# Performance work log

Hardware: AMD Instinct MI355X
Metric: run time of the kernel (lower is better)

Reference implementation:

```python
import jax, jax.numpy as jnp
import numpy as np

B, N, C = 2, 512, 256


def setup_inputs() -> dict:
    key = jax.random.key(0)
    ks = jax.random.split(key, 6)
    s = 0.02
    return {
        "x": jax.random.normal(ks[0], (B, N, C), dtype=jnp.float32),
        "Wq": jax.random.normal(ks[1], (C, C), dtype=jnp.float32) * s,
        "Wk": jax.random.normal(ks[2], (C, C), dtype=jnp.float32) * s,
        "Wv": jax.random.normal(ks[3], (C, C), dtype=jnp.float32) * s,
        "Wp": jax.random.normal(ks[4], (C, C), dtype=jnp.float32) * s,
        "bp": jax.random.normal(ks[5], (C,), dtype=jnp.float32) * s,
    }


def reference(x, Wq, Wk, Wv, Wp, bp):
    # q,k,v: [B,N,C]; torch Linear(no bias) = x @ W.T
    q = jnp.einsum("bnc,dc->bnd", x, Wq)
    k = jnp.einsum("bnc,dc->bnd", x, Wk)
    v = jnp.einsum("bnc,dc->bnd", x, Wv)
    # additive score: sum_c relu(q_i + k_j)  -> [B,N,N]
    score = jax.nn.relu(q[:, :, None, :] + k[:, None, :, :]).sum(axis=-1)
    attn = jax.nn.softmax(score, axis=-1)  # [B,N,N] over keys j
    out = jnp.einsum("bij,bjc->bic", attn, v)  # weighted v sum
    out = jnp.einsum("bnc,dc->bnd", out, Wp) + bp  # proj (with bias)
    return out
```

## Files before the change

kernel.cpp:

```cpp
#include <hip/hip_runtime.h>
#include <hip/hip_bf16.h>


#define QSTR 132
#define VSTR 260

__global__ __launch_bounds__(256, 2) void gemm_qkv(
    const float* __restrict__ x,
    const float* __restrict__ Wq, const float* __restrict__ Wk, const float* __restrict__ Wv,
    float4* __restrict__ qt4, float* __restrict__ k, float* __restrict__ v,
    float* __restrict__ Ksp)
{
    const int z = blockIdx.z;
    const float* W = (z == 0) ? Wq : ((z == 1) ? Wk : Wv);
    const int row0 = blockIdx.x * 32;
    const int d0   = blockIdx.y * 64;

    __shared__ __attribute__((aligned(16))) float AT[2][32][36];
    __shared__ __attribute__((aligned(16))) float WT[2][32][68];

    const int tid = threadIdx.x;
    const int ty = tid >> 4, tx = tid & 15;
    const int ar = tid >> 3, ac = (tid & 7) * 4;
    const int wd = tid >> 2, wc = (tid & 3) * 8;

    const float* xg = x + (size_t)(row0 + ar) * 256 + ac;
    const float* wg = W + (size_t)(d0 + wd) * 256 + wc;

    float4 ra  = *(const float4*)xg;
    float4 rw0 = *(const float4*)wg;
    float4 rw1 = *(const float4*)(wg + 4);

    AT[0][ac+0][ar]=ra.x;  AT[0][ac+1][ar]=ra.y;  AT[0][ac+2][ar]=ra.z;  AT[0][ac+3][ar]=ra.w;
    WT[0][wc+0][wd]=rw0.x; WT[0][wc+1][wd]=rw0.y; WT[0][wc+2][wd]=rw0.z; WT[0][wc+3][wd]=rw0.w;
    WT[0][wc+4][wd]=rw1.x; WT[0][wc+5][wd]=rw1.y; WT[0][wc+6][wd]=rw1.z; WT[0][wc+7][wd]=rw1.w;
    __syncthreads();

    float acc[2][4] = {};

#pragma unroll 1
    for (int kc = 0; kc < 8; ++kc) {
        const int cur = kc & 1;
        if (kc < 7) {
            ra  = *(const float4*)(xg + (kc + 1) * 32);
            rw0 = *(const float4*)(wg + (kc + 1) * 32);
            rw1 = *(const float4*)(wg + (kc + 1) * 32 + 4);
        }
#pragma unroll
        for (int c = 0; c < 32; ++c) {
            float2 a  = *(const float2*)&AT[cur][c][ty * 2];
            float4 w4 = *(const float4*)&WT[cur][c][tx * 4];
            acc[0][0] += a.x * w4.x; acc[0][1] += a.x * w4.y;
            acc[0][2] += a.x * w4.z; acc[0][3] += a.x * w4.w;
            acc[1][0] += a.y * w4.x; acc[1][1] += a.y * w4.y;
            acc[1][2] += a.y * w4.z; acc[1][3] += a.y * w4.w;
        }
        if (kc < 7) {
            const int nx = cur ^ 1;
            AT[nx][ac+0][ar]=ra.x;  AT[nx][ac+1][ar]=ra.y;  AT[nx][ac+2][ar]=ra.z;  AT[nx][ac+3][ar]=ra.w;
            WT[nx][wc+0][wd]=rw0.x; WT[nx][wc+1][wd]=rw0.y; WT[nx][wc+2][wd]=rw0.z; WT[nx][wc+3][wd]=rw0.w;
            WT[nx][wc+4][wd]=rw1.x; WT[nx][wc+5][wd]=rw1.y; WT[nx][wc+6][wd]=rw1.z; WT[nx][wc+7][wd]=rw1.w;
            __syncthreads();
        }
    }

    if (z == 0) {
#pragma unroll
        for (int rr = 0; rr < 2; ++rr)
            qt4[(size_t)(d0 / 4 + tx) * 1024 + row0 + ty * 2 + rr] =
                make_float4(acc[rr][0], acc[rr][1], acc[rr][2], acc[rr][3]);
    } else {
        float* out = (z == 1) ? k : v;
#pragma unroll
        for (int rr = 0; rr < 2; ++rr)
            *(float4*)&out[(size_t)(row0 + ty * 2 + rr) * 256 + d0 + tx * 4] =
                make_float4(acc[rr][0], acc[rr][1], acc[rr][2], acc[rr][3]);
        if (z == 1) {
#pragma unroll
            for (int rr = 0; rr < 2; ++rr) {
                float kp = acc[rr][0] + acc[rr][1] + acc[rr][2] + acc[rr][3];
#pragma unroll
                for (int d = 1; d < 16; d <<= 1) kp += __shfl_xor(kp, d, 16);
                if (tx == 0)
                    Ksp[(size_t)(d0 >> 6) * 1024 + row0 + ty * 2 + rr] = kp;
            }
        }
    }
}

__global__ __launch_bounds__(512) void attn_partial(
    const float4* __restrict__ qt4, const float* __restrict__ kk,
    const float* __restrict__ vv, const float* __restrict__ Ksp,
    float4* __restrict__ pacc4, float* __restrict__ ml)
{
    const int it = blockIdx.x;
    const int js = blockIdx.y;
    const int b  = it >> 3;
    const int irow0 = it * 64;
    const int jrow0 = b * 512 + js * 32;

    __shared__ __attribute__((aligned(16))) float qbuf[64 * QSTR];
    __shared__ __attribute__((aligned(16))) float kbuf[32 * QSTR];
    __shared__ float sL[32][65];
    __shared__ float pl[32][65];

    const int t = threadIdx.x;
    const int w = t >> 6;
    const int l = t & 63;
    const int j0 = w * 4;

    float s[4] = {0.f, 0.f, 0.f, 0.f};

    for (int h = 0; h < 2; ++h) {
#pragma unroll
        for (int u = 0; u < 4; ++u) {
            int idx = u * 512 + t;
            int c4 = idx >> 6, row = idx & 63;
            *(float4*)&qbuf[row * QSTR + c4 * 4] =
                qt4[(size_t)(h * 32 + c4) * 1024 + irow0 + row];
        }
#pragma unroll
        for (int u = 0; u < 2; ++u) {
            int idx = u * 512 + t;
            int row = idx >> 5, c4 = idx & 31;
            *(float4*)&kbuf[row * QSTR + c4 * 4] =
                *(const float4*)&kk[(size_t)(jrow0 + row) * 256 + h * 128 + c4 * 4];
        }
        __syncthreads();

        const float* qrow = &qbuf[l * QSTR];
        const float* k0p = &kbuf[(j0 + 0) * QSTR];
        const float* k1p = &kbuf[(j0 + 1) * QSTR];
        const float* k2p = &kbuf[(j0 + 2) * QSTR];
        const float* k3p = &kbuf[(j0 + 3) * QSTR];

        float4 Aqa,Aqb,Ak0a,Ak0b,Ak1a,Ak1b,Ak2a,Ak2b,Ak3a,Ak3b;
        float4 Bqa,Bqb,Bk0a,Bk0b,Bk1a,Bk1b,Bk2a,Bk2b,Bk3a,Bk3b;

#define LDCH(P, c) \
        P##qa  = *(const float4*)(qrow + (c)); P##qb  = *(const float4*)(qrow + (c) + 4); \
        P##k0a = *(const float4*)(k0p + (c)); P##k0b = *(const float4*)(k0p + (c) + 4); \
        P##k1a = *(const float4*)(k1p + (c)); P##k1b = *(const float4*)(k1p + (c) + 4); \
        P##k2a = *(const float4*)(k2p + (c)); P##k2b = *(const float4*)(k2p + (c) + 4); \
        P##k3a = *(const float4*)(k3p + (c)); P##k3b = *(const float4*)(k3p + (c) + 4);
#define CMPJ(jj, QA, QB, KA, KB) \
        s[jj] += fabsf(QA.x + KA.x); s[jj] += fabsf(QA.y + KA.y); \
        s[jj] += fabsf(QA.z + KA.z); s[jj] += fabsf(QA.w + KA.w); \
        s[jj] += fabsf(QB.x + KB.x); s[jj] += fabsf(QB.y + KB.y); \
        s[jj] += fabsf(QB.z + KB.z); s[jj] += fabsf(QB.w + KB.w);
#define CMPALL(P) \
        CMPJ(0, P##qa, P##qb, P##k0a, P##k0b) CMPJ(1, P##qa, P##qb, P##k1a, P##k1b) \
        CMPJ(2, P##qa, P##qb, P##k2a, P##k2b) CMPJ(3, P##qa, P##qb, P##k3a, P##k3b)

        LDCH(A, 0)
#pragma unroll 1
        for (int c0 = 0; c0 < 128; c0 += 16) {
            LDCH(B, c0 + 8)
            CMPALL(A)
            int cn = (c0 + 16) & 127;
            LDCH(A, cn)
            CMPALL(B)
        }
        __syncthreads();
    }

    const int jbase = jrow0 + j0;
    float sc[4];
#pragma unroll
    for (int jj = 0; jj < 4; ++jj) {
        float ks = Ksp[jbase + jj] + Ksp[1024 + jbase + jj]
                 + Ksp[2048 + jbase + jj] + Ksp[3072 + jbase + jj];
        sc[jj] = 0.5f * (s[jj] + ks);
        sL[j0 + jj][l] = sc[jj];
    }

#pragma unroll
    for (int u = 0; u < 4; ++u) {
        int idx = u * 512 + t;
        int row = idx >> 6, c4 = idx & 63;
        *(float4*)&qbuf[row * VSTR + c4 * 4] =
            *(const float4*)&vv[(size_t)(jrow0 + row) * 256 + c4 * 4];
    }
    __syncthreads();

    float m = -1e30f;
#pragma unroll 8
    for (int j = 0; j < 32; ++j) m = fmaxf(m, sL[j][l]);
#pragma unroll
    for (int jj = 0; jj < 4; ++jj)
        pl[j0 + jj][l] = __expf(sc[jj] - m);
    __syncthreads();

    if (w == 0) {
        float lsum = 0.f;
#pragma unroll 8
        for (int j = 0; j < 32; ++j) lsum += pl[j][l];
        *(float2*)&ml[((size_t)(irow0 + l) * 16 + js) * 2] = make_float2(m, lsum);
    }

#define PVACC(P, V0, V1, V2, V3) \
        acc[0]  += P * V0.x; acc[1]  += P * V0.y; acc[2]  += P * V0.z; acc[3]  += P * V0.w; \
        acc[4]  += P * V1.x; acc[5]  += P * V1.y; acc[6]  += P * V1.z; acc[7]  += P * V1.w; \
        acc[8]  += P * V2.x; acc[9]  += P * V2.y; acc[10] += P * V2.z; acc[11] += P * V2.w; \
        acc[12] += P * V3.x; acc[13] += P * V3.y; acc[14] += P * V3.z; acc[15] += P * V3.w;
#define LDV(P, jj) \
        P##p0 = pl[jj][l];        P##p1 = pl[(jj) + 1][l]; \
        P##v0 = *(const float4*)(vb + (jj) * VSTR);      P##v1 = *(const float4*)(vb + (jj) * VSTR + 4); \
        P##v2 = *(const float4*)(vb + (jj) * VSTR + 8);  P##v3 = *(const float4*)(vb + (jj) * VSTR + 12); \
        P##w0 = *(const float4*)(vb + ((jj)+1) * VSTR);     P##w1 = *(const float4*)(vb + ((jj)+1) * VSTR + 4); \
        P##w2 = *(const float4*)(vb + ((jj)+1) * VSTR + 8); P##w3 = *(const float4*)(vb + ((jj)+1) * VSTR + 12);

#pragma unroll 1
    for (int pass = 0; pass < 2; ++pass) {
        const int cb = w * 32 + pass * 16;
        const float* vb = &qbuf[cb];
        float acc[16];
#pragma unroll
        for (int i = 0; i < 16; ++i) acc[i] = 0.f;

        float Ap0, Ap1, Bp0, Bp1;
        float4 Av0,Av1,Av2,Av3, Aw0,Aw1,Aw2,Aw3;
        float4 Bv0,Bv1,Bv2,Bv3, Bw0,Bw1,Bw2,Bw3;
        LDV(A, 0)
#pragma unroll 1
        for (int j = 0; j < 32; j += 4) {
            LDV(B, j + 2)
            PVACC(Ap0, Av0, Av1, Av2, Av3)
            PVACC(Ap1, Aw0, Aw1, Aw2, Aw3)
            int jn = (j + 4) & 31;
            LDV(A, jn)
            PVACC(Bp0, Bv0, Bv1, Bv2, Bv3)
            PVACC(Bp1, Bw0, Bw1, Bw2, Bw3)
        }
        float4* pout = pacc4 + (((size_t)it * 16 + js) * 64 + (cb >> 2)) * 64 + l;
        pout[0]   = make_float4(acc[0],  acc[1],  acc[2],  acc[3]);
        pout[64]  = make_float4(acc[4],  acc[5],  acc[6],  acc[7]);
        pout[128] = make_float4(acc[8],  acc[9],  acc[10], acc[11]);
        pout[192] = make_float4(acc[12], acc[13], acc[14], acc[15]);
    }
}

__global__ __launch_bounds__(256) void combine(
    const float4* __restrict__ pacc4, const float* __restrict__ ml, float* __restrict__ OT)
{
    const int it = blockIdx.x;
    const int cs = blockIdx.y;
    const int t  = threadIdx.x;
    const int il = t & 63, cq = t >> 6;
    const int row = it * 64 + il;
    const int c4g = cs * 4 + cq;

    float mv[16], lv[16], M = -1e30f;
#pragma unroll
    for (int s = 0; s < 16; ++s) {
        float2 e = *(const float2*)&ml[((size_t)row * 16 + s) * 2];
        mv[s] = e.x; lv[s] = e.y; M = fmaxf(M, e.x);
    }
    float L = 0.f;
    float4 o = make_float4(0.f, 0.f, 0.f, 0.f);
#pragma unroll
    for (int s = 0; s < 16; ++s) {
        float wgt = __expf(mv[s] - M);
        L += wgt * lv[s];
        float4 pv = pacc4[(((size_t)it * 16 + s) * 64 + c4g) * 64 + il];
        o.x += wgt * pv.x; o.y += wgt * pv.y; o.z += wgt * pv.z; o.w += wgt * pv.w;
    }
    float inv = 1.f / L;
    OT[(size_t)(c4g * 4 + 0) * 1024 + row] = o.x * inv;
    OT[(size_t)(c4g * 4 + 1) * 1024 + row] = o.y * inv;
    OT[(size_t)(c4g * 4 + 2) * 1024 + row] = o.z * inv;
    OT[(size_t)(c4g * 4 + 3) * 1024 + row] = o.w * inv;
}

__global__ __launch_bounds__(256, 2) void gemm_bias(
    const float* __restrict__ OT, const float* __restrict__ W,
    const float* __restrict__ bias, float* __restrict__ out)
{
    const int row0 = blockIdx.x * 32;
    const int d0   = blockIdx.y * 64;

    __shared__ __attribute__((aligned(16))) float AT[2][32][36];
    __shared__ __attribute__((aligned(16))) float WT[2][32][68];

    const int tid = threadIdx.x;
    const int ty = tid >> 4, tx = tid & 15;
    const int acR = tid >> 3, arQ = (tid & 7) * 4;
    const int wd = tid >> 2, wc = (tid & 3) * 8;

    const float* ag = OT + (size_t)acR * 1024 + row0 + arQ;
    const float* wg = W + (size_t)(d0 + wd) * 256 + wc;

    float4 ra  = *(const float4*)ag;
    float4 rw0 = *(const float4*)wg;
    float4 rw1 = *(const float4*)(wg + 4);

    *(float4*)&AT[0][acR][arQ] = ra;
    WT[0][wc+0][wd]=rw0.x; WT[0][wc+1][wd]=rw0.y; WT[0][wc+2][wd]=rw0.z; WT[0][wc+3][wd]=rw0.w;
    WT[0][wc+4][wd]=rw1.x; WT[0][wc+5][wd]=rw1.y; WT[0][wc+6][wd]=rw1.z; WT[0][wc+7][wd]=rw1.w;
    __syncthreads();

    float acc[2][4] = {};

#pragma unroll 1
    for (int kc = 0; kc < 8; ++kc) {
        const int cur = kc & 1;
        if (kc < 7) {
            ra  = *(const float4*)(ag + (size_t)(kc + 1) * 32 * 1024);
            rw0 = *(const float4*)(wg + (kc + 1) * 32);
            rw1 = *(const float4*)(wg + (kc + 1) * 32 + 4);
        }
#pragma unroll
        for (int c = 0; c < 32; ++c) {
            float2 a  = *(const float2*)&AT[cur][c][ty * 2];
            float4 w4 = *(const float4*)&WT[cur][c][tx * 4];
            acc[0][0] += a.x * w4.x; acc[0][1] += a.x * w4.y;
            acc[0][2] += a.x * w4.z; acc[0][3] += a.x * w4.w;
            acc[1][0] += a.y * w4.x; acc[1][1] += a.y * w4.y;
            acc[1][2] += a.y * w4.z; acc[1][3] += a.y * w4.w;
        }
        if (kc < 7) {
            const int nx = cur ^ 1;
            *(float4*)&AT[nx][acR][arQ] = ra;
            WT[nx][wc+0][wd]=rw0.x; WT[nx][wc+1][wd]=rw0.y; WT[nx][wc+2][wd]=rw0.z; WT[nx][wc+3][wd]=rw0.w;
            WT[nx][wc+4][wd]=rw1.x; WT[nx][wc+5][wd]=rw1.y; WT[nx][wc+6][wd]=rw1.z; WT[nx][wc+7][wd]=rw1.w;
            __syncthreads();
        }
    }
    float4 bb = *(const float4*)&bias[d0 + tx * 4];
#pragma unroll
    for (int rr = 0; rr < 2; ++rr) {
        float4 o = make_float4(acc[rr][0] + bb.x, acc[rr][1] + bb.y,
                               acc[rr][2] + bb.z, acc[rr][3] + bb.w);
        *(float4*)&out[(size_t)(row0 + ty * 2 + rr) * 256 + d0 + tx * 4] = o;
    }
}

extern "C" void kernel_launch(void* const* d_in, const int* in_sizes, int n_in,
                              void* d_out, int out_size, void* d_ws, size_t ws_size,
                              hipStream_t stream) {
    const float* x  = (const float*)d_in[0];
    const float* Wq = (const float*)d_in[1];
    const float* Wk = (const float*)d_in[2];
    const float* Wv = (const float*)d_in[3];
    const float* Wp = (const float*)d_in[4];
    const float* bp = (const float*)d_in[5];
    float* out = (float*)d_out;
    (void)ws_size; (void)in_sizes; (void)n_in; (void)out_size;

    float* ws = (float*)d_ws;
    const size_t BNC = (size_t)2 * 512 * 256;
    float4* qt4 = (float4*)ws;
    float* k    = ws + BNC;
    float* v    = k + BNC;
    float* OT   = v + BNC;
    float* Ksp  = OT + BNC;
    float4* pacc4 = (float4*)(Ksp + 4 * 1024);
    float* mlb  = (float*)(pacc4 + (size_t)16 * 16 * 64 * 64);

    gemm_qkv<<<dim3(32, 4, 3), 256, 0, stream>>>(x, Wq, Wk, Wv, qt4, k, v, Ksp);
    attn_partial<<<dim3(16, 16), 512, 0, stream>>>(qt4, k, v, Ksp, pacc4, mlb);
    combine<<<dim3(16, 16), 256, 0, stream>>>(pacc4, mlb, OT);
    gemm_bias<<<dim3(32, 4), 256, 0, stream>>>(OT, Wp, bp, out);
}
```

Baseline: 61.14 us.

## Fold output projection into value weights and fuse PV with projection

Precomputes Wvp = Wp·Wv so that the V GEMM directly yields projected values. The attention kernel now writes only normalized-partial probabilities P^T plus max/sum stats, and a new pv_proj kernel applies softmax rescaling on the fly while computing P·Vp plus bias. This removes the separate combine and projection GEMM kernels and the large partial-accumulator buffer. In exchange it adds a small weight GEMM launch per call and a 512x1024 probability matrix round-trip through memory.

Measured after the change: 62.16 us. No clear change (+1.7%).

```diff
diff --git a/kernel.cpp b/kernel.cpp
--- a/kernel.cpp
+++ b/kernel.cpp
@@ -3,16 +3,55 @@
 
 
 #define QSTR 132
-#define VSTR 260
+
+__global__ __launch_bounds__(256) void wvp_gemm(
+    const float* __restrict__ Wp, const float* __restrict__ Wv, float* __restrict__ Wvp)
+{
+    const int row0 = blockIdx.x * 32;
+    const int e0   = blockIdx.y * 64;
+
+    __shared__ __attribute__((aligned(16))) float AT[32][36];
+    __shared__ __attribute__((aligned(16))) float BT[32][68];
+
+    const int t = threadIdx.x;
+    const int ty = t >> 4, tx = t & 15;
+    float acc[2][4] = {};
+
+    for (int c0 = 0; c0 < 256; c0 += 32) {
+        {
+            int r = t >> 3, cb = (t & 7) * 4;
+            float4 a = *(const float4*)&Wp[(size_t)(row0 + r) * 256 + c0 + cb];
+            AT[cb+0][r]=a.x; AT[cb+1][r]=a.y; AT[cb+2][r]=a.z; AT[cb+3][r]=a.w;
+        }
+        {
+            int cc = t >> 3, ec = (t & 7) * 8;
+            *(float4*)&BT[cc][ec]     = *(const float4*)&Wv[(size_t)(c0 + cc) * 256 + e0 + ec];
+            *(float4*)&BT[cc][ec + 4] = *(const float4*)&Wv[(size_t)(c0 + cc) * 256 + e0 + ec + 4];
+        }
+        __syncthreads();
+#pragma unroll
+        for (int c = 0; c < 32; ++c) {
+            float2 a  = *(const float2*)&AT[c][ty * 2];
+            float4 w4 = *(const float4*)&BT[c][tx * 4];
+            acc[0][0]+=a.x*w4.x; acc[0][1]+=a.x*w4.y; acc[0][2]+=a.x*w4.z; acc[0][3]+=a.x*w4.w;
+            acc[1][0]+=a.y*w4.x; acc[1][1]+=a.y*w4.y; acc[1][2]+=a.y*w4.z; acc[1][3]+=a.y*w4.w;
+        }
+        __syncthreads();
+    }
+#pragma unroll
+    for (int rr = 0; rr < 2; ++rr)
+        *(float4*)&Wvp[(size_t)(row0 + ty * 2 + rr) * 256 + e0 + tx * 4] =
+            make_float4(acc[rr][0], acc[rr][1], acc[rr][2], acc[rr][3]);
+}
 
 __global__ __launch_bounds__(256, 2) void gemm_qkv(
     const float* __restrict__ x,
-    const float* __restrict__ Wq, const float* __restrict__ Wk, const float* __restrict__ Wv,
-    float4* __restrict__ qt4, float* __restrict__ k, float* __restrict__ v,
+    const float* __restrict__ Wq, const float* __restrict__ Wk, const float* __restrict__ Wvp,
+    float4* __restrict__ qt4, float* __restrict__ k, float* __restrict__ Vp,
     float* __restrict__ Ksp)
 {
     const int z = blockIdx.z;
-    const float* W = (z == 0) ? Wq : ((z == 1) ? Wk : Wv);
+    const float* W = (z == 0) ? Wq : ((z == 1) ? Wk : Wvp);
     const int row0 = blockIdx.x * 32;
     const int d0   = blockIdx.y * 64;
 
@@ -50,10 +89,8 @@
         for (int c = 0; c < 32; ++c) {
             float2 a  = *(const float2*)&AT[cur][c][ty * 2];
             float4 w4 = *(const float4*)&WT[cur][c][tx * 4];
-            acc[0][0] += a.x * w4.x; acc[0][1] += a.x * w4.y;
-            acc[0][2] += a.x * w4.z; acc[0][3] += a.x * w4.w;
-            acc[1][0] += a.y * w4.x; acc[1][1] += a.y * w4.y;
-            acc[1][2] += a.y * w4.z; acc[1][3] += a.y * w4.w;
+            acc[0][0]+=a.x*w4.x; acc[0][1]+=a.x*w4.y; acc[0][2]+=a.x*w4.z; acc[0][3]+=a.x*w4.w;
+            acc[1][0]+=a.y*w4.x; acc[1][1]+=a.y*w4.y; acc[1][2]+=a.y*w4.z; acc[1][3]+=a.y*w4.w;
         }
         if (kc < 7) {
             const int nx = cur ^ 1;
@@ -70,7 +107,7 @@
             qt4[(size_t)(d0 / 4 + tx) * 1024 + row0 + ty * 2 + rr] =
                 make_float4(acc[rr][0], acc[rr][1], acc[rr][2], acc[rr][3]);
     } else {
-        float* out = (z == 1) ? k : v;
+        float* out = (z == 1) ? k : Vp;
 #pragma unroll
         for (int rr = 0; rr < 2; ++rr)
             *(float4*)&out[(size_t)(row0 + ty * 2 + rr) * 256 + d0 + tx * 4] =
@@ -88,10 +125,9 @@
     }
 }
 
-__global__ __launch_bounds__(512) void attn_partial(
+__global__ __launch_bounds__(512) void attn_score(
     const float4* __restrict__ qt4, const float* __restrict__ kk,
-    const float* __restrict__ vv, const float* __restrict__ Ksp,
-    float4* __restrict__ pacc4, float* __restrict__ ml)
+    const float* __restrict__ Ksp, float* __restrict__ PT, float* __restrict__ ml)
 {
     const int it = blockIdx.x;
     const int js = blockIdx.y;
@@ -101,8 +137,8 @@
 
     __shared__ __attribute__((aligned(16))) float qbuf[64 * QSTR];
     __shared__ __attribute__((aligned(16))) float kbuf[32 * QSTR];
-    __shared__ float sL[32][65];
-    __shared__ float pl[32][65];
+    __shared__ float smax[8][65];
+    __shared__ float psum[8][65];
 
     const int t = threadIdx.x;
     const int w = t >> 6;
@@ -171,168 +207,109 @@
         float ks = Ksp[jbase + jj] + Ksp[1024 + jbase + jj]
                  + Ksp[2048 + jbase + jj] + Ksp[3072 + jbase + jj];
         sc[jj] = 0.5f * (s[jj] + ks);
-        sL[j0 + jj][l] = sc[jj];
-    }
-
-#pragma unroll
-    for (int u = 0; u < 4; ++u) {
-        int idx = u * 512 + t;
-        int row = idx >> 6, c4 = idx & 63;
-        *(float4*)&qbuf[row * VSTR + c4 * 4] =
-            *(const float4*)&vv[(size_t)(jrow0 + row) * 256 + c4 * 4];
-    }
-    __syncthreads();
-
-    float m = -1e30f;
-#pragma unroll 8
-    for (int j = 0; j < 32; ++j) m = fmaxf(m, sL[j][l]);
-#pragma unroll
-    for (int jj = 0; jj < 4; ++jj)
-        pl[j0 + jj][l] = __expf(sc[jj] - m);
+    }
+    smax[w][l] = fmaxf(fmaxf(sc[0], sc[1]), fmaxf(sc[2], sc[3]));
+    __syncthreads();
+
+    float m = smax[0][l];
+#pragma unroll
+    for (int ww = 1; ww < 8; ++ww) m = fmaxf(m, smax[ww][l]);
+
+    float ps = 0.f;
+#pragma unroll
+    for (int jj = 0; jj < 4; ++jj) {
+        float p = __expf(sc[jj] - m);
+        ps += p;
+        PT[(size_t)(js * 32 + j0 + jj) * 1024 + irow0 + l] = p;
+    }
+    psum[w][l] = ps;
     __syncthreads();
 
     if (w == 0) {
         float lsum = 0.f;
-#pragma unroll 8
-        for (int j = 0; j < 32; ++j) lsum += pl[j][l];
+#pragma unroll
+        for (int ww = 0; ww < 8; ++ww) lsum += psum[ww][l];
         *(float2*)&ml[((size_t)(irow0 + l) * 16 + js) * 2] = make_float2(m, lsum);
     }
-
-#define PVACC(P, V0, V1, V2, V3) \
-        acc[0]  += P * V0.x; acc[1]  += P * V0.y; acc[2]  += P * V0.z; acc[3]  += P * V0.w; \
-        acc[4]  += P * V1.x; acc[5]  += P * V1.y; acc[6]  += P * V1.z; acc[7]  += P * V1.w; \
-        acc[8]  += P * V2.x; acc[9]  += P * V2.y; acc[10] += P * V2.z; acc[11] += P * V2.w; \
-        acc[12] += P * V3.x; acc[13] += P * V3.y; acc[14] += P * V3.z; acc[15] += P * V3.w;
-#define LDV(P, jj) \
-        P##p0 = pl[jj][l];        P##p1 = pl[(jj) + 1][l]; \
-        P##v0 = *(const float4*)(vb + (jj) * VSTR);      P##v1 = *(const float4*)(vb + (jj) * VSTR + 4); \
-        P##v2 = *(const float4*)(vb + (jj) * VSTR + 8);  P##v3 = *(const float4*)(vb + (jj) * VSTR + 12); \
-        P##w0 = *(const float4*)(vb + ((jj)+1) * VSTR);     P##w1 = *(const float4*)(vb + ((jj)+1) * VSTR + 4); \
-        P##w2 = *(const float4*)(vb + ((jj)+1) * VSTR + 8); P##w3 = *(const float4*)(vb + ((jj)+1) * VSTR + 12);
+}
+
+__global__ __launch_bounds__(256) void pv_proj(
+    const float* __restrict__ PT, const float* __restrict__ ml,
+    const float* __restrict__ Vp, const float* __restrict__ bias,
+    float* __restrict__ out)
+{
+    const int row0 = blockIdx.x * 16;
+    const int d0   = blockIdx.y * 64;
+    const int b    = row0 >> 9;
+
+    __shared__ float wgtL[16][17];
+    __shared__ __attribute__((aligned(16))) float AT[2][32][18];
+    __shared__ __attribute__((aligned(16))) float BT[2][32][68];
+
+    const int t = threadIdx.x;
+    const int ty = t >> 4, tx = t & 15;
+
+    {
+        int r = t >> 4, s = t & 15;
+        float2 e = *(const float2*)&ml[((size_t)(row0 + r) * 16 + s) * 2];
+        float M = e.x;
+#pragma unroll
+        for (int d = 1; d < 16; d <<= 1) M = fmaxf(M, __shfl_xor(M, d, 16));
+        float ex = __expf(e.x - M);
+        float Lp = ex * e.y;
+#pragma unroll
+        for (int d = 1; d < 16; d <<= 1) Lp += __shfl_xor(Lp, d, 16);
+        wgtL[r][s] = ex / Lp;
+    }
+    __syncthreads();
+
+    const int cc = t >> 3;
+    const int r2 = (t & 7) * 2;
+    const int ec = (t & 7) * 8;
+    const float* ptg = PT + (size_t)cc * 1024 + row0 + r2;
+    const float* vpg = Vp + (size_t)(b * 512 + cc) * 256 + d0 + ec;
+
+    float2 ra  = *(const float2*)ptg;
+    float4 rb0 = *(const float4*)vpg;
+    float4 rb1 = *(const float4*)(vpg + 4);
+    {
+        AT[0][cc][r2]     = ra.x * wgtL[r2][0];
+        AT[0][cc][r2 + 1] = ra.y * wgtL[r2 + 1][0];
+        *(float4*)&BT[0][cc][ec]     = rb0;
+        *(float4*)&BT[0][cc][ec + 4] = rb1;
+    }
+    __syncthreads();
+
+    float acc[4] = {0.f, 0.f, 0.f, 0.f};
 
 #pragma unroll 1
-    for (int pass = 0; pass < 2; ++pass) {
-        const int cb = w * 32 + pass * 16;
-        const float* vb = &qbuf[cb];
-        float acc[16];
-#pragma unroll
-        for (int i = 0; i < 16; ++i) acc[i] = 0.f;
-
-        float Ap0, Ap1, Bp0, Bp1;
-        float4 Av0,Av1,Av2,Av3, Aw0,Aw1,Aw2,Aw3;
-        float4 Bv0,Bv1,Bv2,Bv3, Bw0,Bw1,Bw2,Bw3;
-        LDV(A, 0)
-#pragma unroll 1
-        for (int j = 0; j < 32; j += 4) {
-            LDV(B, j + 2)
-            PVACC(Ap0, Av0, Av1, Av2, Av3)
-            PVACC(Ap1, Aw0, Aw1, Aw2, Aw3)
-            int jn = (j + 4) & 31;
-            LDV(A, jn)
-            PVACC(Bp0, Bv0, Bv1, Bv2, Bv3)
-            PVACC(Bp1, Bw0, Bw1, Bw2, Bw3)
-        }
-        float4* pout = pacc4 + (((size_t)it * 16 + js) * 64 + (cb >> 2)) * 64 + l;
-        pout[0]   = make_float4(acc[0],  acc[1],  acc[2],  acc[3]);
-        pout[64]  = make_float4(acc[4],  acc[5],  acc[6],  acc[7]);
-        pout[128] = make_float4(acc[8],  acc[9],  acc[10], acc[11]);
-        pout[192] = make_float4(acc[12], acc[13], acc[14], acc[15]);
-    }
-}
-
-__global__ __launch_bounds__(256) void combine(
-    const float4* __restrict__ pacc4, const float* __restrict__ ml, float* __restrict__ OT)
-{
-    const int it = blockIdx.x;
-    const int cs = blockIdx.y;
-    const int t  = threadIdx.x;
-    const int il = t & 63, cq = t >> 6;
-    const int row = it * 64 + il;
-    const int c4g = cs * 4 + cq;
-
-    float mv[16], lv[16], M = -1e30f;
-#pragma unroll
-    for (int s = 0; s < 16; ++s) {
-        float2 e = *(const float2*)&ml[((size_t)row * 16 + s) * 2];
-        mv[s] = e.x; lv[s] = e.y; M = fmaxf(M, e.x);
-    }
-    float L = 0.f;
-    float4 o = make_float4(0.f, 0.f, 0.f, 0.f);
-#pragma unroll
-    for (int s = 0; s < 16; ++s) {
-        float wgt = __expf(mv[s] - M);
-        L += wgt * lv[s];
-        float4 pv = pacc4[(((size_t)it * 16 + s) * 64 + c4g) * 64 + il];
-        o.x += wgt * pv.x; o.y += wgt * pv.y; o.z += wgt * pv.z; o.w += wgt * pv.w;
-    }
-    float inv = 1.f / L;
-    OT[(size_t)(c4g * 4 + 0) * 1024 + row] = o.x * inv;
-    OT[(size_t)(c4g * 4 + 1) * 1024 + row] = o.y * inv;
-    OT[(size_t)(c4g * 4 + 2) * 1024 + row] = o.z * inv;
-    OT[(size_t)(c4g * 4 + 3) * 1024 + row] = o.w * inv;
-}
-
-__global__ __launch_bounds__(256, 2) void gemm_bias(
-    const float* __restrict__ OT, const float* __restrict__ W,
-    const float* __restrict__ bias, float* __restrict__ out)
-{
-    const int row0 = blockIdx.x * 32;
-    const int d0   = blockIdx.y * 64;
-
-    __shared__ __attribute__((aligned(16))) float AT[2][32][36];
-    __shared__ __attribute__((aligned(16))) float WT[2][32][68];
-
-    const int tid = threadIdx.x;
-    const int ty = tid >> 4, tx = tid & 15;
-    const int acR = tid >> 3, arQ = (tid & 7) * 4;
-    const int wd = tid >> 2, wc = (tid & 3) * 8;
-
-    const float* ag = OT + (size_t)acR * 1024 + row0 + arQ;
-    const float* wg = W + (size_t)(d0 + wd) * 256 + wc;
-
-    float4 ra  = *(const float4*)ag;
-    float4 rw0 = *(const float4*)wg;
-    float4 rw1 = *(const float4*)(wg + 4);
-
-    *(float4*)&AT[0][acR][arQ] = ra;
-    WT[0][wc+0][wd]=rw0.x; WT[0][wc+1][wd]=rw0.y; WT[0][wc+2][wd]=rw0.z; WT[0][wc+3][wd]=rw0.w;
-    WT[0][wc+4][wd]=rw1.x; WT[0][wc+5][wd]=rw1.y; WT[0][wc+6][wd]=rw1.z; WT[0][wc+7][wd]=rw1.w;
-    __syncthreads();
-
-    float acc[2][4] = {};
-
-#pragma unroll 1
-    for (int kc = 0; kc < 8; ++kc) {
+    for (int kc = 0; kc < 16; ++kc) {
         const int cur = kc & 1;
-        if (kc < 7) {
-            ra  = *(const float4*)(ag + (size_t)(kc + 1) * 32 * 1024);
-            rw0 = *(const float4*)(wg + (kc + 1) * 32);
-            rw1 = *(const float4*)(wg + (kc + 1) * 32 + 4);
+        if (kc < 15) {
+            ra  = *(const float2*)(ptg + (size_t)(kc + 1) * 32 * 1024);
+            rb0 = *(const float4*)(vpg + (size_t)(kc + 1) * 32 * 256);
+            rb1 = *(const float4*)(vpg + (size_t)(kc + 1) * 32 * 256 + 4);
         }
 #pragma unroll
         for (int c = 0; c < 32; ++c) {
-            float2 a  = *(const float2*)&AT[cur][c][ty * 2];
-            float4 w4 = *(const float4*)&WT[cur][c][tx * 4];
-            acc[0][0] += a.x * w4.x; acc[0][1] += a.x * w4.y;
-            acc[0][2] += a.x * w4.z; acc[0][3] += a.x * w4.w;
-            acc[1][0] += a.y * w4.x; acc[1][1] += a.y * w4.y;
-            acc[1][2] += a.y * w4.z; acc[1][3] += a.y * w4.w;
-        }
-        if (kc < 7) {
+            float a   = AT[cur][c][ty];
+            float4 w4 = *(const float4*)&BT[cur][c][tx * 4];
+            acc[0] += a * w4.x; acc[1] += a * w4.y;
+            acc[2] += a * w4.z; acc[3] += a * w4.w;
+        }
+        if (kc < 15) {
             const int nx = cur ^ 1;
-            *(float4*)&AT[nx][acR][arQ] = ra;
-            WT[nx][wc+0][wd]=rw0.x; WT[nx][wc+1][wd]=rw0.y; WT[nx][wc+2][wd]=rw0.z; WT[nx][wc+3][wd]=rw0.w;
-            WT[nx][wc+4][wd]=rw1.x; WT[nx][wc+5][wd]=rw1.y; WT[nx][wc+6][wd]=rw1.z; WT[nx][wc+7][wd]=rw1.w;
+            AT[nx][cc][r2]     = ra.x * wgtL[r2][kc + 1];
+            AT[nx][cc][r2 + 1] = ra.y * wgtL[r2 + 1][kc + 1];
+            *(float4*)&BT[nx][cc][ec]     = rb0;
+            *(float4*)&BT[nx][cc][ec + 4] = rb1;
             __syncthreads();
         }
     }
+
     float4 bb = *(const float4*)&bias[d0 + tx * 4];
-#pragma unroll
-    for (int rr = 0; rr < 2; ++rr) {
-        float4 o = make_float4(acc[rr][0] + bb.x, acc[rr][1] + bb.y,
-                               acc[rr][2] + bb.z, acc[rr][3] + bb.w);
-        *(float4*)&out[(size_t)(row0 + ty * 2 + rr) * 256 + d0 + tx * 4] = o;
-    }
+    *(float4*)&out[(size_t)(row0 + ty) * 256 + d0 + tx * 4] =
+        make_float4(acc[0] + bb.x, acc[1] + bb.y, acc[2] + bb.z, acc[3] + bb.w);
 }
 
 extern "C" void kernel_launch(void* const* d_in, const int* in_sizes, int n_in,
@@ -351,14 +328,14 @@
     const size_t BNC = (size_t)2 * 512 * 256;
     float4* qt4 = (float4*)ws;
     float* k    = ws + BNC;
-    float* v    = k + BNC;
-    float* OT   = v + BNC;
-    float* Ksp  = OT + BNC;
-    float4* pacc4 = (float4*)(Ksp + 4 * 1024);
-    float* mlb  = (float*)(pacc4 + (size_t)16 * 16 * 64 * 64);
-
-    gemm_qkv<<<dim3(32, 4, 3), 256, 0, stream>>>(x, Wq, Wk, Wv, qt4, k, v, Ksp);
-    attn_partial<<<dim3(16, 16), 512, 0, stream>>>(qt4, k, v, Ksp, pacc4, mlb);
-    combine<<<dim3(16, 16), 256, 0, stream>>>(pacc4, mlb, OT);
-    gemm_bias<<<dim3(32, 4), 256, 0, stream>>>(OT, Wp, bp, out);
-}
+    float* Vp   = k + BNC;
+    float* Ksp  = Vp + BNC;
+    float* PT   = Ksp + 4 * 1024;
+    float* mlb  = PT + (size_t)512 * 1024;
+    float* Wvp  = mlb + (size_t)1024 * 16 * 2;
+
+    wvp_gemm<<<dim3(8, 4), 256, 0, stream>>>(Wp, Wv, Wvp);
+    gemm_qkv<<<dim3(32, 4, 3), 256, 0, stream>>>(x, Wq, Wk, Wvp, qt4, k, Vp, Ksp);
+    attn_score<<<dim3(16, 16), 512, 0, stream>>>(qt4, k, Ksp, PT, mlb);
+    pv_proj<<<dim3(64, 4), 256, 0, stream>>>(PT, mlb, Vp, bp, out);
+}
```
